# Optimization experiments

Hardware: AMD Instinct MI355X
Metric: run time of the kernel (lower is better)

## Reference

```python
import jax, jax.numpy as jnp
import numpy as np

PAD_IDX = 1  # word2vec key_to_index['<PAD>'] / padding_idx in the original
VOCAB, EMBED, HIDDEN, SEQ = 100000, 300, 512, 1024


def setup_inputs() -> dict:
    key = jax.random.key(0)
    k = jax.random.split(key, 8)
    s = 1.0 / np.sqrt(HIDDEN)  # PyTorch LSTM init scale
    return {
        "input_seq": jax.random.randint(k[0], (1, SEQ), 0, VOCAB, dtype=jnp.int64)
                     if jax.config.jax_enable_x64 else
                     jax.random.randint(k[0], (1, SEQ), 0, VOCAB, dtype=jnp.int32),
        "h0": jnp.zeros((1, 1, HIDDEN), jnp.float32),
        "c0": jnp.zeros((1, 1, HIDDEN), jnp.float32),
        "emb": jax.random.normal(k[1], (VOCAB, EMBED), jnp.float32),  # frozen word2vec table
        "W_ih": jax.random.uniform(k[2], (4 * HIDDEN, EMBED), jnp.float32, -s, s),
        "W_hh": jax.random.uniform(k[3], (4 * HIDDEN, HIDDEN), jnp.float32, -s, s),
        "b_ih": jax.random.uniform(k[4], (4 * HIDDEN,), jnp.float32, -s, s),
        "b_hh": jax.random.uniform(k[5], (4 * HIDDEN,), jnp.float32, -s, s),
    }


def _lstm_scan(xs, is_pad, h, c, W_ih, W_hh, b_ih, b_hh):
    # xs: [S, E]; PAD steps leave (h, c, out) untouched, matching the `continue`.
    x_gates = xs @ W_ih.T + b_ih  # [S, 4H] -- hoist input projection out of the scan
    H = h.shape[-1]

    def step(carry, inp):
        h, c, out = carry
        xg, pad = inp
        g = xg + h @ W_hh.T + b_hh                 # [4H], PyTorch gate order i,f,g,o
        i, f, gg, o = jnp.split(g, 4)
        c_new = jax.nn.sigmoid(f) * c + jax.nn.sigmoid(i) * jnp.tanh(gg)
        h_new = jax.nn.sigmoid(o) * jnp.tanh(c_new)
        h = jnp.where(pad, h, h_new)
        c = jnp.where(pad, c, c_new)
        out = jnp.where(pad, out, h_new)
        return (h, c, out), None

    (h, c, out), _ = jax.lax.scan(step, (h, c, jnp.zeros(H, xs.dtype)), (x_gates, is_pad))
    return h, c, out


def reference(input_seq, h0, c0, emb, W_ih, W_hh, b_ih, b_hh):
    tokens = input_seq[0]                 # batch==1 in the original
    xs = emb[tokens]                      # [S, E] embedding gather (fused into recurrence)
    is_pad = tokens == PAD_IDX
    h, c, out = _lstm_scan(xs, is_pad, h0[0, 0], c0[0, 0], W_ih, W_hh, b_ih, b_hh)
    # original returns output=None if every token is PAD; here out stays zeros.
    return (out[None, None, :], (h[None, None, :], c[None, None, :]))
```

## Files before the change

### kernel.cpp

```cpp
#include <hip/hip_runtime.h>
#include <hip/hip_cooperative_groups.h>
#include <math.h>

#define SEQ    1024
#define EMBED  300
#define HIDDEN 512
#define NB     128
#define NBLK   256
#define TPB    256
#define UPB    (HIDDEN/NB)
#define PAD_IDX 1
#define SENT   0x7FC00BADu

#define HSLOT  32
#define HROW   (NB * HSLOT)

__device__ __align__(128) float g_hp[(SEQ + 1) * HROW];
__device__ unsigned int g_done;
__device__ float        g_sink;

__device__ __forceinline__ float sigmoidf_(float x) {
    return 1.f / (1.f + __expf(-x));
}
__device__ __forceinline__ float tanhf_(float x) {
    return 1.f - 2.f / (__expf(2.f * x) + 1.f);
}

#define DPP_ADD(v, ctrl)                                                      \
    (v) += __int_as_float(__builtin_amdgcn_update_dpp(                        \
        0, __float_as_int(v), (ctrl), 0xf, 0xf, true))

__global__ __launch_bounds__(TPB, 1) void fused_kernel(
    const int* __restrict__ seq, const float* __restrict__ h0,
    const float* __restrict__ c0, const float* __restrict__ emb,
    const float* __restrict__ W_ih, const float* __restrict__ Whh,
    const float* __restrict__ b_ih, const float* __restrict__ b_hh,
    float* __restrict__ out)
{
    const int b = blockIdx.x, tid = threadIdx.x;
    const int gid = b * TPB + tid;

    for (int i = gid; i < (SEQ + 1) * NB * UPB; i += NBLK * TPB) {
        int step = i >> 9;
        int w    = i & 511;
        int blk  = w >> 2, k = w & 3;
        float v = __uint_as_float(SENT);
        if (step == 0) v = h0[blk * UPB + k];
        g_hp[(size_t)step * HROW + blk * HSLOT + k] = v;
    }
    if (gid == 0) g_done = 0u;

    cooperative_groups::this_grid().sync();

    if (b >= NB) {
        if (tid < 128) {
            float a0 = 1.0f + tid, a1 = 2.0f, a2 = 3.0f, a3 = 4.0f;
            for (;;) {
                #pragma unroll
                for (int i = 0; i < 128; i++) {
                    a0 = fmaf(a0, 1.000001f, 0.5f);
                    a1 = fmaf(a1, 0.999999f, 0.25f);
                    a2 = fmaf(a2, 1.0000005f, a0);
                    a3 = fmaf(a3, 0.9999995f, a1);
                }
                if (__hip_atomic_load(&g_done, __ATOMIC_RELAXED,
                                      __HIP_MEMORY_SCOPE_AGENT)) break;
            }
            if (a0 == 1234.5678f && a1 == a2) g_sink = a3;
        }
        return;
    }

    const int u = tid >> 6;
    const int lane = tid & 63;
    const int g = lane >> 4, c = lane & 15;
    const int U = b * UPB + u;
    const int R = g * HIDDEN + U;

    const float* wrow = Whh + (size_t)R * HIDDEN + c * 32;
    float4 wreg[8];
    #pragma unroll
    for (int i = 0; i < 8; i++) {
        int off = (4 * i + 4 * c) & 31;
        wreg[i] = *(const float4*)(wrow + off);
    }

    float4 wih[5];
    #pragma unroll
    for (int j = 0; j < 5; j++) wih[j] = make_float4(0.f, 0.f, 0.f, 0.f);
    if (c < 15) {
        const float* xr = W_ih + (size_t)R * EMBED + c * 20;
        #pragma unroll
        for (int j = 0; j < 5; j++) wih[j] = *(const float4*)(xr + 4 * j);
    }
    const bool gate_lane = (c == 0);
    float bias = 0.f;
    if (gate_lane) bias = b_ih[R] + b_hh[R];

    __shared__ __align__(16) float h_lds[2][HIDDEN];
    __shared__ int tok_lds[SEQ];

    for (int i = tid; i < SEQ; i += TPB) tok_lds[i] = seq[i];

    const bool owner = (lane == 0);
    float c_state = 0.f, h_state = 0.f;
    if (owner) {
        c_state = c0[U];
        h_state = h0[U];
    }
    __syncthreads();

    float4 er[5];
    #pragma unroll
    for (int j = 0; j < 5; j++) er[j] = make_float4(0.f, 0.f, 0.f, 0.f);
    {
        int tf = 0;
        while (tf < SEQ && tok_lds[tf] == PAD_IDX) tf++;
        if (tf < SEQ && c < 15) {
            const float* ep = emb + (size_t)tok_lds[tf] * EMBED + c * 20;
            #pragma unroll
            for (int j = 0; j < 5; j++) er[j] = *(const float4*)(ep + 4 * j);
        }
    }

    int np = 0;
    bool any = false;

    for (int t = 0; t < SEQ; t++) {
        int tok = tok_lds[t];
        if (tok == PAD_IDX) continue;
        any = true;

        float ix = 0.f;
        #pragma unroll
        for (int j = 0; j < 5; j++) {
            ix = fmaf(wih[j].x, er[j].x, ix);
            ix = fmaf(wih[j].y, er[j].y, ix);
            ix = fmaf(wih[j].z, er[j].z, ix);
            ix = fmaf(wih[j].w, er[j].w, ix);
        }
        int tn = t + 1;
        while (tn < SEQ && tok_lds[tn] == PAD_IDX) tn++;
        if (tn < SEQ && c < 15) {
            const float* ep = emb + (size_t)tok_lds[tn] * EMBED + c * 20;
            #pragma unroll
            for (int j = 0; j < 5; j++) er[j] = *(const float4*)(ep + 4 * j);
        }

        if (tid < NB) {
            const unsigned long long* hb_ =
                (const unsigned long long*)(g_hp + (size_t)np * HROW + tid * HSLOT);
            unsigned long long p0, p1;
            for (;;) {
                p0 = __hip_atomic_load(hb_ + 0, __ATOMIC_RELAXED,
                                       __HIP_MEMORY_SCOPE_AGENT);
                p1 = __hip_atomic_load(hb_ + 1, __ATOMIC_RELAXED,
                                       __HIP_MEMORY_SCOPE_AGENT);
                if ((unsigned)p0 != SENT && (unsigned)(p0 >> 32) != SENT &&
                    (unsigned)p1 != SENT && (unsigned)(p1 >> 32) != SENT)
                    break;
            }
            unsigned long long* dst =
                (unsigned long long*)&h_lds[np & 1][tid * UPB];
            dst[0] = p0; dst[1] = p1;
        }
        __syncthreads();

        const float* hc = h_lds[np & 1] + c * 32;
        float4 a4 = {0.f, 0.f, 0.f, 0.f};
        #pragma unroll
        for (int i = 0; i < 8; i++) {
            int off = (4 * i + 4 * c) & 31;
            float4 h4 = *(const float4*)(hc + off);
            a4.x = fmaf(wreg[i].x, h4.x, a4.x);
            a4.y = fmaf(wreg[i].y, h4.y, a4.y);
            a4.z = fmaf(wreg[i].z, h4.z, a4.z);
            a4.w = fmaf(wreg[i].w, h4.w, a4.w);
        }
        float dotv = (a4.x + a4.y) + (a4.z + a4.w) + ix;
        DPP_ADD(dotv, 0xB1);
        DPP_ADD(dotv, 0x4E);
        DPP_ADD(dotv, 0x141);
        DPP_ADD(dotv, 0x140);

        float act = 0.f;
        if (gate_lane) {
            float z = dotv + bias;
            act = (g == 2) ? tanhf_(z) : sigmoidf_(z);
        }
        float fv = __shfl(act, 16);
        float gv = __shfl(act, 32);
        float ov = __shfl(act, 48);

        if (owner) {
            c_state = fv * c_state + act * gv;
            h_state = ov * tanhf_(c_state);
            __hip_atomic_store(
                (unsigned*)(g_hp + (size_t)(np + 1) * HROW + b * HSLOT) + u,
                __float_as_uint(h_state),
                __ATOMIC_RELAXED, __HIP_MEMORY_SCOPE_AGENT);
        }
        np++;
    }

    if (owner) {
        out[U]              = any ? h_state : 0.f;
        out[HIDDEN + U]     = h_state;
        out[2 * HIDDEN + U] = c_state;
    }
    if (b == 0 && tid == 0) {
        __hip_atomic_store(&g_done, 1u, __ATOMIC_RELAXED,
                           __HIP_MEMORY_SCOPE_AGENT);
    }
}

extern "C" void kernel_launch(void* const* d_in, const int* in_sizes, int n_in,
                              void* d_out, int out_size, void* d_ws, size_t ws_size,
                              hipStream_t stream)
{
    const int*   seq  = (const int*)  d_in[0];
    const float* h0   = (const float*)d_in[1];
    const float* c0   = (const float*)d_in[2];
    const float* emb  = (const float*)d_in[3];
    const float* W_ih = (const float*)d_in[4];
    const float* W_hh = (const float*)d_in[5];
    const float* b_ih = (const float*)d_in[6];
    const float* b_hh = (const float*)d_in[7];
    float* out = (float*)d_out;

    void* args[] = { (void*)&seq, (void*)&h0, (void*)&c0, (void*)&emb,
                     (void*)&W_ih, (void*)&W_hh, (void*)&b_ih, (void*)&b_hh,
                     (void*)&out };
    hipLaunchCooperativeKernel((const void*)fused_kernel, dim3(NBLK), dim3(TPB),
                               args, 0, stream);
}
```

Measured before the change: 1.843 ms.

## Stage embedding rows through LDS ring buffer and prefetch two steps ahead

```diff
diff --git a/kernel.cpp b/kernel.cpp
--- a/kernel.cpp
+++ b/kernel.cpp
@@ -29,6 +29,19 @@
 #define DPP_ADD(v, ctrl)                                                      \
     (v) += __int_as_float(__builtin_amdgcn_update_dpp(                        \
         0, __float_as_int(v), (ctrl), 0xf, 0xf, true))
+
+__device__ __forceinline__ float ixdot(const float* er, const float4* wih) {
+    float x0 = 0.f, x1 = 0.f, x2 = 0.f, x3 = 0.f;
+    #pragma unroll
+    for (int j = 0; j < 5; j++) {
+        float4 e4 = *(const float4*)(er + 4 * j);
+        x0 = fmaf(wih[j].x, e4.x, x0);
+        x1 = fmaf(wih[j].y, e4.y, x1);
+        x2 = fmaf(wih[j].z, e4.z, x2);
+        x3 = fmaf(wih[j].w, e4.w, x3);
+    }
+    return (x0 + x1) + (x2 + x3);
+}
 
 __global__ __launch_bounds__(TPB, 1) void fused_kernel(
     const int* __restrict__ seq, const float* __restrict__ h0,
@@ -98,6 +111,7 @@
     if (gate_lane) bias = b_ih[R] + b_hh[R];
 
     __shared__ __align__(16) float h_lds[2][HIDDEN];
+    __shared__ __align__(16) float ering[4][320];
     __shared__ int tok_lds[SEQ];
 
     for (int i = tid; i < SEQ; i += TPB) tok_lds[i] = seq[i];
@@ -110,18 +124,21 @@
     }
     __syncthreads();
 
-    float4 er[5];
-    #pragma unroll
-    for (int j = 0; j < 5; j++) er[j] = make_float4(0.f, 0.f, 0.f, 0.f);
-    {
-        int tf = 0;
-        while (tf < SEQ && tok_lds[tf] == PAD_IDX) tf++;
-        if (tf < SEQ && c < 15) {
-            const float* ep = emb + (size_t)tok_lds[tf] * EMBED + c * 20;
-            #pragma unroll
-            for (int j = 0; j < 5; j++) er[j] = *(const float4*)(ep + 4 * j);
-        }
-    }
+    int rt0 = 0;
+    while (rt0 < SEQ && tok_lds[rt0] == PAD_IDX) rt0++;
+    int rt1 = (rt0 < SEQ) ? rt0 + 1 : SEQ;
+    while (rt1 < SEQ && tok_lds[rt1] == PAD_IDX) rt1++;
+
+    if (rt0 < SEQ && tid < 75)
+        *(float4*)&ering[0][4 * tid] =
+            *(const float4*)(emb + (size_t)tok_lds[rt0] * EMBED + 4 * tid);
+    if (rt1 < SEQ && tid >= 128 && tid < 203)
+        *(float4*)&ering[1][4 * (tid - 128)] =
+            *(const float4*)(emb + (size_t)tok_lds[rt1] * EMBED + 4 * (tid - 128));
+    __syncthreads();
+
+    float ixc = ixdot(&ering[0][c * 20], wih);
+    int tpre = (rt1 < SEQ) ? rt1 : SEQ;
 
     int np = 0;
     bool any = false;
@@ -130,22 +147,6 @@
         int tok = tok_lds[t];
         if (tok == PAD_IDX) continue;
         any = true;
-
-        float ix = 0.f;
-        #pragma unroll
-        for (int j = 0; j < 5; j++) {
-            ix = fmaf(wih[j].x, er[j].x, ix);
-            ix = fmaf(wih[j].y, er[j].y, ix);
-            ix = fmaf(wih[j].z, er[j].z, ix);
-            ix = fmaf(wih[j].w, er[j].w, ix);
-        }
-        int tn = t + 1;
-        while (tn < SEQ && tok_lds[tn] == PAD_IDX) tn++;
-        if (tn < SEQ && c < 15) {
-            const float* ep = emb + (size_t)tok_lds[tn] * EMBED + c * 20;
-            #pragma unroll
-            for (int j = 0; j < 5; j++) er[j] = *(const float4*)(ep + 4 * j);
-        }
 
         if (tid < NB) {
             const unsigned long long* hb_ =
@@ -166,6 +167,23 @@
         }
         __syncthreads();
 
+        float4 ev = make_float4(0.f, 0.f, 0.f, 0.f);
+        bool pf = false;
+        const int pidx = tid - 128;
+        if (tid >= 128) {
+            int tn = tpre + 1;
+            while (tn < SEQ && tok_lds[tn] == PAD_IDX) tn++;
+            if (tn < SEQ) {
+                if (pidx < 75)
+                    ev = *(const float4*)(emb + (size_t)tok_lds[tn] * EMBED
+                                          + 4 * pidx);
+                pf = true;
+                tpre = tn;
+            } else {
+                tpre = SEQ;
+            }
+        }
+
         const float* hc = h_lds[np & 1] + c * 32;
         float4 a4 = {0.f, 0.f, 0.f, 0.f};
         #pragma unroll
@@ -177,11 +195,16 @@
             a4.z = fmaf(wreg[i].z, h4.z, a4.z);
             a4.w = fmaf(wreg[i].w, h4.w, a4.w);
         }
-        float dotv = (a4.x + a4.y) + (a4.z + a4.w) + ix;
+        float dotv = (a4.x + a4.y) + (a4.z + a4.w) + ixc;
         DPP_ADD(dotv, 0xB1);
         DPP_ADD(dotv, 0x4E);
         DPP_ADD(dotv, 0x141);
         DPP_ADD(dotv, 0x140);
+
+        ixc = ixdot(&ering[(np + 1) & 3][c * 20], wih);
+
+        if (pf && pidx < 75)
+            *(float4*)&ering[(np + 2) & 3][4 * pidx] = ev;
 
         float act = 0.f;
         if (gate_lane) {
```

New measurement: 2.916 ms. 58.2% more time.
